# Optimization experiments

Measured on AMD Instinct MI355X. Metric: run time of the kernel, lower is better.

Reference implementation:

```python
import jax, jax.numpy as jnp
import numpy as np

NUM_USERS = 100000
NUM_ITEMS = 50000
EMB = 64
E_U = 1200000
E_I = 600000


def setup_inputs() -> dict:
    key = jax.random.key(0)
    k1, k2, k3, k4 = jax.random.split(key, 4)
    return {
        "user_edge_index": jax.random.randint(k1, (2, E_U), 0, NUM_USERS, dtype=jnp.int32),
        "item_edge_index": jax.random.randint(k2, (2, E_I), 0, NUM_ITEMS, dtype=jnp.int32),
        "W_user": jax.random.normal(k3, (NUM_USERS, EMB), dtype=jnp.float32) * 0.1,
        "b_user": jnp.zeros((EMB,), dtype=jnp.float32),
        "W_item": jax.random.normal(k4, (NUM_ITEMS, EMB), dtype=jnp.float32) * 0.1,
        "b_item": jnp.zeros((EMB,), dtype=jnp.float32),
    }


def _gcn(W, b, edge_index, n):
    # x = I, so x @ kernel == kernel (W).  GCN renorm: relu(D^-1/2 (A+I) D^-1/2 W + b)
    self_loops = jnp.arange(n, dtype=edge_index.dtype)
    row = jnp.concatenate([edge_index[0], self_loops])
    col = jnp.concatenate([edge_index[1], self_loops])
    deg = jax.ops.segment_sum(jnp.ones(row.shape[0], dtype=W.dtype), row, num_segments=n)
    inv_sqrt = jnp.where(deg > 0, jax.lax.rsqrt(jnp.maximum(deg, 1e-12)), 0.0)
    norm = inv_sqrt[row] * inv_sqrt[col]           # [E+n]
    msgs = W[col] * norm[:, None]                  # gather + scale: [E+n, EMB]
    agg = jax.ops.segment_sum(msgs, row, num_segments=n)  # scatter-add: [n, EMB]
    return jax.nn.relu(agg + b)


def reference(user_edge_index, item_edge_index, W_user, b_user, W_item, b_item):
    user_h = _gcn(W_user, b_user, user_edge_index, NUM_USERS)
    item_h = _gcn(W_item, b_item, item_edge_index, NUM_ITEMS)
    return (user_h, item_h)
```

## Files before the change

kernel.cpp:

```cpp
#include <hip/hip_runtime.h>
#include <hip/hip_fp16.h>

#define NUSERS 100000
#define NITEMS 50000
#define EMB 64
#define BROWS 1024
#define CHUNK 4096
#define MAXB 128
#define CAP  16384
#define NB_U ((NUSERS + BROWS - 1) / BROWS)
#define NB_I ((NITEMS + BROWS - 1) / BROWS)


__global__ void bscatter2_kernel(const int* __restrict__ rowU, const int* __restrict__ rowI,
                                 unsigned* __restrict__ bcntU, unsigned* __restrict__ bcntI,
                                 unsigned* __restrict__ pairsU, unsigned* __restrict__ pairsI,
                                 int EU, int EI, int gbU) {
    __shared__ unsigned h[MAXB];
    __shared__ unsigned base[MAXB];
    __shared__ int rstage[CHUNK];
    const int* row; const int* col; unsigned* bcnt; unsigned* pairs; int E, blk, nb;
    if ((int)blockIdx.x < gbU) { row = rowU; col = rowU + EU; bcnt = bcntU; pairs = pairsU; E = EU; blk = blockIdx.x; nb = NB_U; }
    else                       { row = rowI; col = rowI + EI; bcnt = bcntI; pairs = pairsI; E = EI; blk = blockIdx.x - gbU; nb = NB_I; }
    int t = threadIdx.x;
    for (int i = t; i < nb; i += blockDim.x) h[i] = 0;
    __syncthreads();
    int lo = blk * CHUNK, hi = min(lo + CHUNK, E);
    for (int i = lo + t; i < hi; i += blockDim.x) {
        int r = row[i];
        rstage[i - lo] = r;
        atomicAdd(&h[r >> 10], 1u);
    }
    __syncthreads();
    for (int i = t; i < nb; i += blockDim.x) {
        unsigned cnt = h[i];
        base[i] = cnt ? ((unsigned)i * CAP + atomicAdd(&bcnt[i], cnt)) : 0u;
        h[i] = 0;
    }
    __syncthreads();
    for (int i = lo + t; i < hi; i += blockDim.x) {
        int r = rstage[i - lo];
        int b = r >> 10;
        unsigned p = base[b] + atomicAdd(&h[b], 1u);
        pairs[p] = ((unsigned)(r & 1023) << 20) | (unsigned)col[i];
    }
}

__global__ void bprep_kernel(const unsigned* __restrict__ bcntU, const unsigned* __restrict__ bcntI,
                             const unsigned* __restrict__ pairsU, const unsigned* __restrict__ pairsI,
                             uint2* __restrict__ odU, uint2* __restrict__ odI,
                             float* __restrict__ invU, float* __restrict__ invI,
                             int* __restrict__ colsU, int* __restrict__ colsI,
                             unsigned* __restrict__ totU, unsigned* __restrict__ totI) {
    __shared__ unsigned d[BROWS];
    __shared__ unsigned c[BROWS];
    __shared__ unsigned sh[256];
    __shared__ unsigned sbase;
    const unsigned* bcnt; const unsigned* pairs; uint2* od; float* inv; int* cols; unsigned* tot; int n, b;
    if ((int)blockIdx.x < NB_U) { bcnt = bcntU; pairs = pairsU; od = odU; inv = invU; cols = colsU; tot = totU; n = NUSERS; b = blockIdx.x; }
    else                        { bcnt = bcntI; pairs = pairsI; od = odI; inv = invI; cols = colsI; tot = totI; n = NITEMS; b = blockIdx.x - NB_U; }
    int t = threadIdx.x;
    int rbase = b * BROWS;
    for (int i = t; i < BROWS; i += 256) d[i] = 0;
    __syncthreads();
    unsigned lo = (unsigned)b * CAP, hi = lo + bcnt[b];
    for (unsigned i = lo + t; i < hi; i += 256)
        atomicAdd(&d[pairs[i] >> 20], 1u);
    __syncthreads();
    unsigned v[4], s = 0;
    #pragma unroll
    for (int i = 0; i < 4; i++) { v[i] = d[t * 4 + i]; s += v[i]; }
    sh[t] = s;
    __syncthreads();
    for (int off = 1; off < 256; off <<= 1) {
        unsigned add = (t >= off) ? sh[t - off] : 0u;
        __syncthreads();
        sh[t] += add;
        __syncthreads();
    }
    if (t == 255) sbase = atomicAdd(tot, sh[255]);
    __syncthreads();
    unsigned running = sbase + sh[t] - s;
    #pragma unroll
    for (int i = 0; i < 4; i++) {
        int li = t * 4 + i;
        int idx = rbase + li;
        if (idx < n) {
            od[idx] = make_uint2(running, v[i]);
            inv[idx] = rsqrtf((float)(v[i] + 1u));
            c[li] = running;
            running += v[i];
        }
    }
    __syncthreads();
    for (unsigned i = lo + t; i < hi; i += 256) {
        unsigned pk = pairs[i];
        unsigned p = atomicAdd(&c[pk >> 20], 1u);
        cols[p] = (int)(pk & 0xFFFFFu);
    }
}

__global__ void tohalf2_kernel(const float* __restrict__ WU, const float* __restrict__ WI,
                               const float* __restrict__ invU, const float* __restrict__ invI,
                               __half* __restrict__ WhU, __half* __restrict__ WhI) {
    const int totU = NUSERS * EMB / 4;
    const int totI = NITEMS * EMB / 4;
    int i = blockIdx.x * 256 + threadIdx.x;
    const float* W; const float* inv; __half* Wh;
    if (i < totU)             { W = WU; inv = invU; Wh = WhU; }
    else if (i < totU + totI) { i -= totU; W = WI; inv = invI; Wh = WhI; }
    else return;
    int r = i >> 4;
    float s = inv[r];
    float4 w = ((const float4*)W)[i];
    __half2 h0 = __floats2half2_rn(w.x * s, w.y * s);
    __half2 h1 = __floats2half2_rn(w.z * s, w.w * s);
    ((__half2*)Wh)[2 * i]     = h0;
    ((__half2*)Wh)[2 * i + 1] = h1;
}

__device__ __forceinline__ void acc8(float* acc, float4 f) {
    const __half2* h = (const __half2*)&f;
    #pragma unroll
    for (int j = 0; j < 4; j++) {
        float2 tv = __half22float2(h[j]);
        acc[2 * j]     += tv.x;
        acc[2 * j + 1] += tv.y;
    }
}

__global__ void gather2h_kernel(const uint2* __restrict__ odU, const uint2* __restrict__ odI,
                                const int* __restrict__ colsU, const int* __restrict__ colsI,
                                const __half* __restrict__ WhU, const __half* __restrict__ WhI,
                                const float* __restrict__ bU, const float* __restrict__ bI,
                                const float* __restrict__ invU, const float* __restrict__ invI,
                                float* __restrict__ outU, float* __restrict__ outI, int ggU) {
    const uint2* od; const int* cols; const __half* Wh; const float* bb; const float* inv;
    float* out; int n, r0;
    if ((int)blockIdx.x < ggU) { od = odU; cols = colsU; Wh = WhU; bb = bU; inv = invU; out = outU; n = NUSERS; r0 = blockIdx.x * 32; }
    else                       { od = odI; cols = colsI; Wh = WhI; bb = bI; inv = invI; out = outI; n = NITEMS; r0 = (blockIdx.x - ggU) * 32; }
    int r = r0 + (threadIdx.x >> 3);
    if (r >= n) return;
    int d8 = threadIdx.x & 7;
    uint2 o = od[r];
    unsigned k = o.x, end = o.x + o.y;
    const __half* wb = Wh + d8 * 8;
    float acc[8] = {0.f, 0.f, 0.f, 0.f, 0.f, 0.f, 0.f, 0.f};
    for (; k + 4 <= end; k += 4) {
        int c0 = cols[k];
        int c1 = cols[k + 1];
        int c2 = cols[k + 2];
        int c3 = cols[k + 3];
        float4 f0 = *(const float4*)(wb + (size_t)c0 * EMB);
        float4 f1 = *(const float4*)(wb + (size_t)c1 * EMB);
        float4 f2 = *(const float4*)(wb + (size_t)c2 * EMB);
        float4 f3 = *(const float4*)(wb + (size_t)c3 * EMB);
        acc8(acc, f0); acc8(acc, f1); acc8(acc, f2); acc8(acc, f3);
    }
    for (; k < end; ++k) {
        int c0 = cols[k];
        float4 f0 = *(const float4*)(wb + (size_t)c0 * EMB);
        acc8(acc, f0);
    }
    float inv_r = inv[r];
    float4 fs = *(const float4*)(Wh + (size_t)r * EMB + d8 * 8);
    float sf[8];
    {
        const __half2* h = (const __half2*)&fs;
        #pragma unroll
        for (int j = 0; j < 4; j++) {
            float2 tv = __half22float2(h[j]);
            sf[2 * j] = tv.x; sf[2 * j + 1] = tv.y;
        }
    }
    const float4 bv0 = *(const float4*)(bb + d8 * 8);
    const float4 bv1 = *(const float4*)(bb + d8 * 8 + 4);
    float4 o0, o1;
    o0.x = fmaxf((acc[0] + sf[0]) * inv_r + bv0.x, 0.f);
    o0.y = fmaxf((acc[1] + sf[1]) * inv_r + bv0.y, 0.f);
    o0.z = fmaxf((acc[2] + sf[2]) * inv_r + bv0.z, 0.f);
    o0.w = fmaxf((acc[3] + sf[3]) * inv_r + bv0.w, 0.f);
    o1.x = fmaxf((acc[4] + sf[4]) * inv_r + bv1.x, 0.f);
    o1.y = fmaxf((acc[5] + sf[5]) * inv_r + bv1.y, 0.f);
    o1.z = fmaxf((acc[6] + sf[6]) * inv_r + bv1.z, 0.f);
    o1.w = fmaxf((acc[7] + sf[7]) * inv_r + bv1.w, 0.f);
    *(float4*)(out + (size_t)r * EMB + d8 * 8)     = o0;
    *(float4*)(out + (size_t)r * EMB + d8 * 8 + 4) = o1;
}

__global__ void gather2f_kernel(const uint2* __restrict__ odU, const uint2* __restrict__ odI,
                                const int* __restrict__ colsU, const int* __restrict__ colsI,
                                const float* __restrict__ WU, const float* __restrict__ WI,
                                const float* __restrict__ bU, const float* __restrict__ bI,
                                const float* __restrict__ invU, const float* __restrict__ invI,
                                float* __restrict__ outU, float* __restrict__ outI, int ggU) {
    const uint2* od; const int* cols; const float* W; const float* bb; const float* inv;
    float* out; int n, r0;
    if ((int)blockIdx.x < ggU) { od = odU; cols = colsU; W = WU; bb = bU; inv = invU; out = outU; n = NUSERS; r0 = blockIdx.x * 32; }
    else                       { od = odI; cols = colsI; W = WI; bb = bI; inv = invI; out = outI; n = NITEMS; r0 = (blockIdx.x - ggU) * 32; }
    int r = r0 + (threadIdx.x >> 3);
    if (r >= n) return;
    int d8 = threadIdx.x & 7;
    uint2 o = od[r];
    unsigned k = o.x, end = o.x + o.y;
    const float* wb = W + d8 * 8;
    float acc[8] = {0.f, 0.f, 0.f, 0.f, 0.f, 0.f, 0.f, 0.f};
    for (; k < end; ++k) {
        int c0 = cols[k];
        float ic = inv[c0];
        float4 f0 = *(const float4*)(wb + (size_t)c0 * EMB);
        float4 f1 = *(const float4*)(wb + (size_t)c0 * EMB + 4);
        acc[0] += f0.x * ic; acc[1] += f0.y * ic; acc[2] += f0.z * ic; acc[3] += f0.w * ic;
        acc[4] += f1.x * ic; acc[5] += f1.y * ic; acc[6] += f1.z * ic; acc[7] += f1.w * ic;
    }
    float inv_r = inv[r];
    float4 s0 = *(const float4*)(W + (size_t)r * EMB + d8 * 8);
    float4 s1 = *(const float4*)(W + (size_t)r * EMB + d8 * 8 + 4);
    const float4 bv0 = *(const float4*)(bb + d8 * 8);
    const float4 bv1 = *(const float4*)(bb + d8 * 8 + 4);
    float4 o0, o1;
    o0.x = fmaxf((acc[0] + s0.x * inv_r) * inv_r + bv0.x, 0.f);
    o0.y = fmaxf((acc[1] + s0.y * inv_r) * inv_r + bv0.y, 0.f);
    o0.z = fmaxf((acc[2] + s0.z * inv_r) * inv_r + bv0.z, 0.f);
    o0.w = fmaxf((acc[3] + s0.w * inv_r) * inv_r + bv0.w, 0.f);
    o1.x = fmaxf((acc[4] + s1.x * inv_r) * inv_r + bv1.x, 0.f);
    o1.y = fmaxf((acc[5] + s1.y * inv_r) * inv_r + bv1.y, 0.f);
    o1.z = fmaxf((acc[6] + s1.z * inv_r) * inv_r + bv1.z, 0.f);
    o1.w = fmaxf((acc[7] + s1.w * inv_r) * inv_r + bv1.w, 0.f);
    *(float4*)(out + (size_t)r * EMB + d8 * 8)     = o0;
    *(float4*)(out + (size_t)r * EMB + d8 * 8 + 4) = o1;
}

extern "C" void kernel_launch(void* const* d_in, const int* in_sizes, int n_in,
                              void* d_out, int out_size, void* d_ws, size_t ws_size,
                              hipStream_t stream) {
    const int*   ue = (const int*)d_in[0];
    const int*   ie = (const int*)d_in[1];
    const float* Wu = (const float*)d_in[2];
    const float* bu = (const float*)d_in[3];
    const float* Wi = (const float*)d_in[4];
    const float* bi = (const float*)d_in[5];

    const int E_U = in_sizes[0] / 2;
    const int E_I = in_sizes[1] / 2;

    float* out_u = (float*)d_out;
    float* out_i = out_u + (size_t)NUSERS * EMB;

    unsigned* w       = (unsigned*)d_ws;
    unsigned* bcnt_u  = w;            w += MAXB;
    unsigned* bcnt_i  = w;            w += MAXB;
    unsigned* tot_u   = w;            w += 1;
    unsigned* tot_i   = w;            w += 1;
    uint2*    od_u    = (uint2*)w;    w += 2 * (size_t)NUSERS;
    uint2*    od_i    = (uint2*)w;    w += 2 * (size_t)NITEMS;
    float*    inv_u   = (float*)w;    w += NUSERS;
    float*    inv_i   = (float*)w;    w += NITEMS;
    int*      cols_u  = (int*)w;      w += E_U;
    int*      cols_i  = (int*)w;      w += E_I;
    w += (size_t)(-(intptr_t)(w - (unsigned*)d_ws)) & 3;
    unsigned* un      = w;
    unsigned* pairs_u = un;
    unsigned* pairs_i = un + (size_t)NB_U * CAP;
    __half*   wh_u    = (__half*)un;
    __half*   wh_i    = (__half*)un + (size_t)NUSERS * EMB;
    size_t un_words_pairs = (size_t)(NB_U + NB_I) * CAP;
    size_t un_words_wh    = (size_t)(NUSERS + NITEMS) * EMB / 2;
    size_t un_words = un_words_pairs > un_words_wh ? un_words_pairs : un_words_wh;
    const size_t need_bytes = (size_t)((char*)(un + un_words) - (char*)d_ws);
    const bool use_half = (ws_size >= need_bytes);

    hipMemsetAsync(bcnt_u, 0, (2 * MAXB + 2) * sizeof(unsigned), stream);

    const int gb_u = (E_U + CHUNK - 1) / CHUNK;
    const int gb_i = (E_I + CHUNK - 1) / CHUNK;
    const int gg_u = (NUSERS + 31) / 32;
    const int gg_i = (NITEMS + 31) / 32;

    bscatter2_kernel<<<gb_u + gb_i, 256, 0, stream>>>(ue, ie, bcnt_u, bcnt_i,
                                                      pairs_u, pairs_i, E_U, E_I, gb_u);
    bprep_kernel    <<<NB_U + NB_I, 256, 0, stream>>>(bcnt_u, bcnt_i, pairs_u, pairs_i,
                                                      od_u, od_i, inv_u, inv_i,
                                                      cols_u, cols_i, tot_u, tot_i);
    if (use_half) {
        const int tot4 = (NUSERS + NITEMS) * EMB / 4;
        tohalf2_kernel <<<(tot4 + 255) / 256, 256, 0, stream>>>(Wu, Wi, inv_u, inv_i, wh_u, wh_i);
        gather2h_kernel<<<gg_u + gg_i, 256, 0, stream>>>(od_u, od_i, cols_u, cols_i,
                                                         wh_u, wh_i, bu, bi, inv_u, inv_i,
                                                         out_u, out_i, gg_u);
    } else {
        gather2f_kernel<<<gg_u + gg_i, 256, 0, stream>>>(od_u, od_i, cols_u, cols_i,
                                                         Wu, Wi, bu, bi, inv_u, inv_i,
                                                         out_u, out_i, gg_u);
    }
}
```

Measured before the change: 129.7 us.

## Fuse half conversion into edge bucketing kernel and apply source norm in gather

The fp32-to-fp16 conversion of W no longer depends on the inverse-sqrt degrees, so it runs as extra blocks inside the edge bucketing kernel when the workspace has room for both buffers. The source-node normalisation moves into the gather loop as a per-edge scalar load. Buckets shrink to 512 rows so the bucket prep kernel can stage its pairs in shared memory instead of reading them from global memory twice. The cost is an extra inv[] gather per edge and a per-bucket cap of 8192 edges, which relies on random rows staying under that cap.

```diff
diff --git a/kernel.cpp b/kernel.cpp
--- a/kernel.cpp
+++ b/kernel.cpp
@@ -4,45 +4,61 @@
 #define NUSERS 100000
 #define NITEMS 50000
 #define EMB 64
-#define BROWS 1024
+#define BROWS 512
 #define CHUNK 4096
-#define MAXB 128
-#define CAP  16384
+#define MAXB 256
+#define CAP  8192
+#define NTOH 1024
 #define NB_U ((NUSERS + BROWS - 1) / BROWS)
 #define NB_I ((NITEMS + BROWS - 1) / BROWS)
 
 
-__global__ void bscatter2_kernel(const int* __restrict__ rowU, const int* __restrict__ rowI,
-                                 unsigned* __restrict__ bcntU, unsigned* __restrict__ bcntI,
-                                 unsigned* __restrict__ pairsU, unsigned* __restrict__ pairsI,
-                                 int EU, int EI, int gbU) {
+__global__ void build1_kernel(const int* __restrict__ rowU, const int* __restrict__ rowI,
+                              unsigned* __restrict__ bcntU, unsigned* __restrict__ bcntI,
+                              unsigned* __restrict__ pairsU, unsigned* __restrict__ pairsI,
+                              const float* __restrict__ WU, const float* __restrict__ WI,
+                              __half* __restrict__ WhU, __half* __restrict__ WhI,
+                              int EU, int EI, int gbU, int gbTot) {
     __shared__ unsigned h[MAXB];
     __shared__ unsigned base[MAXB];
     __shared__ int rstage[CHUNK];
-    const int* row; const int* col; unsigned* bcnt; unsigned* pairs; int E, blk, nb;
-    if ((int)blockIdx.x < gbU) { row = rowU; col = rowU + EU; bcnt = bcntU; pairs = pairsU; E = EU; blk = blockIdx.x; nb = NB_U; }
-    else                       { row = rowI; col = rowI + EI; bcnt = bcntI; pairs = pairsI; E = EI; blk = blockIdx.x - gbU; nb = NB_I; }
     int t = threadIdx.x;
-    for (int i = t; i < nb; i += blockDim.x) h[i] = 0;
+    if ((int)blockIdx.x >= gbTot) {
+        int nt = (int)gridDim.x - gbTot;
+        const int T4U = NUSERS * (EMB / 4), T4I = NITEMS * (EMB / 4);
+        for (int i = ((int)blockIdx.x - gbTot) * 256 + t; i < T4U + T4I; i += nt * 256) {
+            const float4* W; __half2* Wh2; int idx;
+            if (i < T4U) { W = (const float4*)WU; Wh2 = (__half2*)WhU; idx = i; }
+            else         { W = (const float4*)WI; Wh2 = (__half2*)WhI; idx = i - T4U; }
+            float4 w = W[idx];
+            Wh2[2 * idx]     = __floats2half2_rn(w.x, w.y);
+            Wh2[2 * idx + 1] = __floats2half2_rn(w.z, w.w);
+        }
+        return;
+    }
+    const int* row; const int* col; unsigned* bcnt; unsigned* pairs; int E, blk;
+    if ((int)blockIdx.x < gbU) { row = rowU; col = rowU + EU; bcnt = bcntU; pairs = pairsU; E = EU; blk = blockIdx.x; }
+    else                       { row = rowI; col = rowI + EI; bcnt = bcntI; pairs = pairsI; E = EI; blk = blockIdx.x - gbU; }
+    for (int i = t; i < MAXB; i += 256) h[i] = 0;
     __syncthreads();
     int lo = blk * CHUNK, hi = min(lo + CHUNK, E);
-    for (int i = lo + t; i < hi; i += blockDim.x) {
+    for (int i = lo + t; i < hi; i += 256) {
         int r = row[i];
         rstage[i - lo] = r;
-        atomicAdd(&h[r >> 10], 1u);
-    }
-    __syncthreads();
-    for (int i = t; i < nb; i += blockDim.x) {
+        atomicAdd(&h[r >> 9], 1u);
+    }
+    __syncthreads();
+    for (int i = t; i < MAXB; i += 256) {
         unsigned cnt = h[i];
         base[i] = cnt ? ((unsigned)i * CAP + atomicAdd(&bcnt[i], cnt)) : 0u;
         h[i] = 0;
     }
     __syncthreads();
-    for (int i = lo + t; i < hi; i += blockDim.x) {
+    for (int i = lo + t; i < hi; i += 256) {
         int r = rstage[i - lo];
-        int b = r >> 10;
+        int b = r >> 9;
         unsigned p = base[b] + atomicAdd(&h[b], 1u);
-        pairs[p] = ((unsigned)(r & 1023) << 20) | (unsigned)col[i];
+        pairs[p] = ((unsigned)(r & 511) << 20) | (unsigned)col[i];
     }
 }
 
@@ -53,8 +69,9 @@
                              int* __restrict__ colsU, int* __restrict__ colsI,
                              unsigned* __restrict__ totU, unsigned* __restrict__ totI) {
     __shared__ unsigned d[BROWS];
-    __shared__ unsigned c[BROWS];
+    __shared__ unsigned cur[BROWS];
     __shared__ unsigned sh[256];
+    __shared__ unsigned stage[CAP];
     __shared__ unsigned sbase;
     const unsigned* bcnt; const unsigned* pairs; uint2* od; float* inv; int* cols; unsigned* tot; int n, b;
     if ((int)blockIdx.x < NB_U) { bcnt = bcntU; pairs = pairsU; od = odU; inv = invU; cols = colsU; tot = totU; n = NUSERS; b = blockIdx.x; }
@@ -63,13 +80,16 @@
     int rbase = b * BROWS;
     for (int i = t; i < BROWS; i += 256) d[i] = 0;
     __syncthreads();
-    unsigned lo = (unsigned)b * CAP, hi = lo + bcnt[b];
-    for (unsigned i = lo + t; i < hi; i += 256)
-        atomicAdd(&d[pairs[i] >> 20], 1u);
-    __syncthreads();
-    unsigned v[4], s = 0;
-    #pragma unroll
-    for (int i = 0; i < 4; i++) { v[i] = d[t * 4 + i]; s += v[i]; }
+    unsigned cnt = min(bcnt[b], (unsigned)CAP);
+    unsigned lo = (unsigned)b * CAP;
+    for (unsigned i = t; i < cnt; i += 256) {
+        unsigned pk = pairs[lo + i];
+        stage[i] = pk;
+        atomicAdd(&d[pk >> 20], 1u);
+    }
+    __syncthreads();
+    unsigned v0 = d[2 * t], v1 = d[2 * t + 1];
+    unsigned s = v0 + v1;
     sh[t] = s;
     __syncthreads();
     for (int off = 1; off < 256; off <<= 1) {
@@ -81,51 +101,37 @@
     if (t == 255) sbase = atomicAdd(tot, sh[255]);
     __syncthreads();
     unsigned running = sbase + sh[t] - s;
-    #pragma unroll
-    for (int i = 0; i < 4; i++) {
-        int li = t * 4 + i;
-        int idx = rbase + li;
-        if (idx < n) {
-            od[idx] = make_uint2(running, v[i]);
-            inv[idx] = rsqrtf((float)(v[i] + 1u));
-            c[li] = running;
-            running += v[i];
-        }
-    }
-    __syncthreads();
-    for (unsigned i = lo + t; i < hi; i += 256) {
-        unsigned pk = pairs[i];
-        unsigned p = atomicAdd(&c[pk >> 20], 1u);
+    int i0 = rbase + 2 * t, i1 = i0 + 1;
+    if (i0 < n) { od[i0] = make_uint2(running, v0); inv[i0] = rsqrtf((float)(v0 + 1u)); cur[2 * t]     = running; running += v0; }
+    if (i1 < n) { od[i1] = make_uint2(running, v1); inv[i1] = rsqrtf((float)(v1 + 1u)); cur[2 * t + 1] = running; running += v1; }
+    __syncthreads();
+    for (unsigned i = t; i < cnt; i += 256) {
+        unsigned pk = stage[i];
+        unsigned p = atomicAdd(&cur[pk >> 20], 1u);
         cols[p] = (int)(pk & 0xFFFFFu);
     }
 }
 
-__global__ void tohalf2_kernel(const float* __restrict__ WU, const float* __restrict__ WI,
-                               const float* __restrict__ invU, const float* __restrict__ invI,
-                               __half* __restrict__ WhU, __half* __restrict__ WhI) {
-    const int totU = NUSERS * EMB / 4;
-    const int totI = NITEMS * EMB / 4;
-    int i = blockIdx.x * 256 + threadIdx.x;
-    const float* W; const float* inv; __half* Wh;
-    if (i < totU)             { W = WU; inv = invU; Wh = WhU; }
-    else if (i < totU + totI) { i -= totU; W = WI; inv = invI; Wh = WhI; }
-    else return;
-    int r = i >> 4;
-    float s = inv[r];
-    float4 w = ((const float4*)W)[i];
-    __half2 h0 = __floats2half2_rn(w.x * s, w.y * s);
-    __half2 h1 = __floats2half2_rn(w.z * s, w.w * s);
-    ((__half2*)Wh)[2 * i]     = h0;
-    ((__half2*)Wh)[2 * i + 1] = h1;
-}
-
-__device__ __forceinline__ void acc8(float* acc, float4 f) {
+__global__ void tohalf_kernel(const float* __restrict__ WU, const float* __restrict__ WI,
+                              __half* __restrict__ WhU, __half* __restrict__ WhI) {
+    const int T4U = NUSERS * (EMB / 4), T4I = NITEMS * (EMB / 4);
+    for (int i = blockIdx.x * 256 + threadIdx.x; i < T4U + T4I; i += gridDim.x * 256) {
+        const float4* W; __half2* Wh2; int idx;
+        if (i < T4U) { W = (const float4*)WU; Wh2 = (__half2*)WhU; idx = i; }
+        else         { W = (const float4*)WI; Wh2 = (__half2*)WhI; idx = i - T4U; }
+        float4 w = W[idx];
+        Wh2[2 * idx]     = __floats2half2_rn(w.x, w.y);
+        Wh2[2 * idx + 1] = __floats2half2_rn(w.z, w.w);
+    }
+}
+
+__device__ __forceinline__ void accs(float* acc, float4 f, float ic) {
     const __half2* h = (const __half2*)&f;
     #pragma unroll
     for (int j = 0; j < 4; j++) {
         float2 tv = __half22float2(h[j]);
-        acc[2 * j]     += tv.x;
-        acc[2 * j + 1] += tv.y;
+        acc[2 * j]     += tv.x * ic;
+        acc[2 * j + 1] += tv.y * ic;
     }
 }
 
@@ -151,39 +157,33 @@
         int c1 = cols[k + 1];
         int c2 = cols[k + 2];
         int c3 = cols[k + 3];
+        float i0 = inv[c0], i1 = inv[c1], i2 = inv[c2], i3 = inv[c3];
         float4 f0 = *(const float4*)(wb + (size_t)c0 * EMB);
         float4 f1 = *(const float4*)(wb + (size_t)c1 * EMB);
         float4 f2 = *(const float4*)(wb + (size_t)c2 * EMB);
         float4 f3 = *(const float4*)(wb + (size_t)c3 * EMB);
-        acc8(acc, f0); acc8(acc, f1); acc8(acc, f2); acc8(acc, f3);
+        accs(acc, f0, i0); accs(acc, f1, i1); accs(acc, f2, i2); accs(acc, f3, i3);
     }
     for (; k < end; ++k) {
         int c0 = cols[k];
+        float i0 = inv[c0];
         float4 f0 = *(const float4*)(wb + (size_t)c0 * EMB);
-        acc8(acc, f0);
+        accs(acc, f0, i0);
     }
     float inv_r = inv[r];
     float4 fs = *(const float4*)(Wh + (size_t)r * EMB + d8 * 8);
-    float sf[8];
-    {
-        const __half2* h = (const __half2*)&fs;
-        #pragma unroll
-        for (int j = 0; j < 4; j++) {
-            float2 tv = __half22float2(h[j]);
-            sf[2 * j] = tv.x; sf[2 * j + 1] = tv.y;
-        }
-    }
+    accs(acc, fs, inv_r);
     const float4 bv0 = *(const float4*)(bb + d8 * 8);
     const float4 bv1 = *(const float4*)(bb + d8 * 8 + 4);
     float4 o0, o1;
-    o0.x = fmaxf((acc[0] + sf[0]) * inv_r + bv0.x, 0.f);
-    o0.y = fmaxf((acc[1] + sf[1]) * inv_r + bv0.y, 0.f);
-    o0.z = fmaxf((acc[2] + sf[2]) * inv_r + bv0.z, 0.f);
-    o0.w = fmaxf((acc[3] + sf[3]) * inv_r + bv0.w, 0.f);
-    o1.x = fmaxf((acc[4] + sf[4]) * inv_r + bv1.x, 0.f);
-    o1.y = fmaxf((acc[5] + sf[5]) * inv_r + bv1.y, 0.f);
-    o1.z = fmaxf((acc[6] + sf[6]) * inv_r + bv1.z, 0.f);
-    o1.w = fmaxf((acc[7] + sf[7]) * inv_r + bv1.w, 0.f);
+    o0.x = fmaxf(acc[0] * inv_r + bv0.x, 0.f);
+    o0.y = fmaxf(acc[1] * inv_r + bv0.y, 0.f);
+    o0.z = fmaxf(acc[2] * inv_r + bv0.z, 0.f);
+    o0.w = fmaxf(acc[3] * inv_r + bv0.w, 0.f);
+    o1.x = fmaxf(acc[4] * inv_r + bv1.x, 0.f);
+    o1.y = fmaxf(acc[5] * inv_r + bv1.y, 0.f);
+    o1.z = fmaxf(acc[6] * inv_r + bv1.z, 0.f);
+    o1.w = fmaxf(acc[7] * inv_r + bv1.w, 0.f);
     *(float4*)(out + (size_t)r * EMB + d8 * 8)     = o0;
     *(float4*)(out + (size_t)r * EMB + d8 * 8 + 4) = o1;
 }
@@ -259,36 +259,52 @@
     int*      cols_u  = (int*)w;      w += E_U;
     int*      cols_i  = (int*)w;      w += E_I;
     w += (size_t)(-(intptr_t)(w - (unsigned*)d_ws)) & 3;
-    unsigned* un      = w;
-    unsigned* pairs_u = un;
-    unsigned* pairs_i = un + (size_t)NB_U * CAP;
-    __half*   wh_u    = (__half*)un;
-    __half*   wh_i    = (__half*)un + (size_t)NUSERS * EMB;
-    size_t un_words_pairs = (size_t)(NB_U + NB_I) * CAP;
-    size_t un_words_wh    = (size_t)(NUSERS + NITEMS) * EMB / 2;
-    size_t un_words = un_words_pairs > un_words_wh ? un_words_pairs : un_words_wh;
-    const size_t need_bytes = (size_t)((char*)(un + un_words) - (char*)d_ws);
-    const bool use_half = (ws_size >= need_bytes);
+
+    const size_t pairs_words = (size_t)(NB_U + NB_I) * CAP;
+    const size_t wh_words    = (size_t)(NUSERS + NITEMS) * EMB / 2;
+    unsigned* pairs_u = w;
+    unsigned* pairs_i = w + (size_t)NB_U * CAP;
+    const size_t need_A = (size_t)((char*)(w + pairs_words + wh_words) - (char*)d_ws);
+    const size_t need_B = (size_t)((char*)(w + (pairs_words > wh_words ? pairs_words : wh_words)) - (char*)d_ws);
+    const bool pathA = (ws_size >= need_A);
+    const bool pathB = (!pathA && ws_size >= need_B);
+    __half* wh_u = pathA ? (__half*)(w + pairs_words) : (__half*)w;
+    __half* wh_i = wh_u + (size_t)NUSERS * EMB;
 
     hipMemsetAsync(bcnt_u, 0, (2 * MAXB + 2) * sizeof(unsigned), stream);
 
-    const int gb_u = (E_U + CHUNK - 1) / CHUNK;
-    const int gb_i = (E_I + CHUNK - 1) / CHUNK;
-    const int gg_u = (NUSERS + 31) / 32;
-    const int gg_i = (NITEMS + 31) / 32;
-
-    bscatter2_kernel<<<gb_u + gb_i, 256, 0, stream>>>(ue, ie, bcnt_u, bcnt_i,
-                                                      pairs_u, pairs_i, E_U, E_I, gb_u);
-    bprep_kernel    <<<NB_U + NB_I, 256, 0, stream>>>(bcnt_u, bcnt_i, pairs_u, pairs_i,
-                                                      od_u, od_i, inv_u, inv_i,
-                                                      cols_u, cols_i, tot_u, tot_i);
-    if (use_half) {
-        const int tot4 = (NUSERS + NITEMS) * EMB / 4;
-        tohalf2_kernel <<<(tot4 + 255) / 256, 256, 0, stream>>>(Wu, Wi, inv_u, inv_i, wh_u, wh_i);
+    const int gb_u  = (E_U + CHUNK - 1) / CHUNK;
+    const int gb_i  = (E_I + CHUNK - 1) / CHUNK;
+    const int gbTot = gb_u + gb_i;
+    const int gg_u  = (NUSERS + 31) / 32;
+    const int gg_i  = (NITEMS + 31) / 32;
+
+    if (pathA) {
+        build1_kernel <<<gbTot + NTOH, 256, 0, stream>>>(ue, ie, bcnt_u, bcnt_i, pairs_u, pairs_i,
+                                                         Wu, Wi, wh_u, wh_i, E_U, E_I, gb_u, gbTot);
+        bprep_kernel  <<<NB_U + NB_I, 256, 0, stream>>>(bcnt_u, bcnt_i, pairs_u, pairs_i,
+                                                        od_u, od_i, inv_u, inv_i,
+                                                        cols_u, cols_i, tot_u, tot_i);
+        gather2h_kernel<<<gg_u + gg_i, 256, 0, stream>>>(od_u, od_i, cols_u, cols_i,
+                                                         wh_u, wh_i, bu, bi, inv_u, inv_i,
+                                                         out_u, out_i, gg_u);
+    } else if (pathB) {
+        build1_kernel <<<gbTot, 256, 0, stream>>>(ue, ie, bcnt_u, bcnt_i, pairs_u, pairs_i,
+                                                  Wu, Wi, wh_u, wh_i, E_U, E_I, gb_u, gbTot);
+        bprep_kernel  <<<NB_U + NB_I, 256, 0, stream>>>(bcnt_u, bcnt_i, pairs_u, pairs_i,
+                                                        od_u, od_i, inv_u, inv_i,
+                                                        cols_u, cols_i, tot_u, tot_i);
+        tohalf_kernel <<<2048, 256, 0, stream>>>(Wu, Wi, wh_u, wh_i);
         gather2h_kernel<<<gg_u + gg_i, 256, 0, stream>>>(od_u, od_i, cols_u, cols_i,
                                                          wh_u, wh_i, bu, bi, inv_u, inv_i,
                                                          out_u, out_i, gg_u);
     } else {
+        build1_kernel <<<gbTot, 256, 0, stream>>>(ue, ie, bcnt_u, bcnt_i, pairs_u, pairs_i,
+                                                  Wu, Wi, (__half*)nullptr, (__half*)nullptr,
+                                                  E_U, E_I, gb_u, gbTot);
+        bprep_kernel  <<<NB_U + NB_I, 256, 0, stream>>>(bcnt_u, bcnt_i, pairs_u, pairs_i,
+                                                        od_u, od_i, inv_u, inv_i,
+                                                        cols_u, cols_i, tot_u, tot_i);
         gather2f_kernel<<<gg_u + gg_i, 256, 0, stream>>>(od_u, od_i, cols_u, cols_i,
                                                          Wu, Wi, bu, bi, inv_u, inv_i,
                                                          out_u, out_i, gg_u);
```

Measured after the change: 116.8 us. -9.9%, faster.
